# Performance work log

Measured on AMD Instinct MI355X. Metric: run time of the kernel, lower is better.

## Reference

```python
import jax, jax.numpy as jnp
import numpy as np

N = 8_388_608        # cohort size (2^23)
T_MAX = 1_000_000    # distinct time values -> ~8 ties per unique time


def setup_inputs() -> dict:
    key = jax.random.key(0)
    k1, k2, k3 = jax.random.split(key, 3)
    x = jax.random.normal(k1, (N,), dtype=jnp.float32)  # risk scores
    times = jax.random.randint(k2, (N,), 0, T_MAX).astype(jnp.float32)
    events = (jax.random.uniform(k3, (N,)) < 0.7).astype(jnp.float32)
    target = jnp.stack([times, events], axis=1)  # [N, 2] = [time, event]
    return {"input": x, "target": target}


def _cox_breslow_sqrt_loss(x, target):
    times = target[:, 0]
    events_all = target[:, 1]
    n = x.shape[0]
    # Sort by descending time (risk set = prefix in this ordering).
    sort_idx = jnp.argsort(-times)
    t = times[sort_idx]
    ev = events_all[sort_idx]
    xs = x[sort_idx]
    # Stable prefix log-sum-exp over the risk set.
    log_cum = jax.lax.cumlogsumexp(xs)
    # end_idx[i] = last index of the tie group containing i (groups are
    # contiguous after sorting). Reverse running-min over positions of
    # group-last elements.
    is_last = jnp.concatenate([t[:-1] != t[1:], jnp.ones((1,), dtype=bool)])
    pos = jnp.where(is_last, jnp.arange(n), n)
    end_idx = jnp.flip(jax.lax.cummin(jnp.flip(pos)))
    # Breslow: -sum(x*ev) + sum_groups logcum[group_end] * (#events in group)
    #        == -sum((x - logcum[end_idx]) * ev)
    loss = -jnp.sum((xs - log_cum[end_idx]) * ev)
    # reduction='mean' -> sqrt(loss / n)
    return jnp.sqrt(loss / n)


def reference(input, target):
    return _cox_breslow_sqrt_loss(input, target)
```

## Files before the change

### kernel.cpp

```cpp
#include <hip/hip_runtime.h>
#include <math.h>

#define TMAX 1000000
#define BINW 4096
#define BINSHIFT 12
#define NBIN 245
#define PADN (NBIN * BINW)
#define TILE 8192
#define NTHR 512
#define CAP 36864
#define CURSOR_STRIDE 16
#define BT_STRIDE 8
#define FIXSCALE 65536.0f
#define INV_FIXSCALE (1.0 / 65536.0)

#define OFF_SCAL     0
#define OFF_DONE     16
#define OFF_CURSOR   64
#define OFF_BINTOT   15744
#define OFF_PAYLOAD  31488
#define MEMSET_BYTES 31424
#define NEED_FULL    ((size_t)OFF_PAYLOAD + (size_t)NBIN * CAP * 4)
#define FB_BINTOT    15744
#define FB_CEXCL     17792
#define FB_BEXP      31488
#define FB_BEV       (FB_BEXP + PADN * 4)
#define NEED_MIN     ((size_t)FB_BEV + PADN * 4)

__device__ __forceinline__ int clamp_tau(float t) {
    int tau = (int)t;
    if (tau < 0) tau = 0;
    if (tau >= TMAX) tau = TMAX - 1;
    return tau;
}

__device__ __forceinline__ unsigned enc_payload(float xv, float tv, float ev_f,
                                                int* bin_out, float* exq_out) {
    int tau = clamp_tau(tv);
    *bin_out = tau >> BINSHIFT;
    int fine = tau & (BINW - 1);
    float ex = __expf(xv);
    unsigned bb = __float_as_uint(ex);
    bb = (bb + 0x7FFFu + ((bb >> 16) & 1u)) >> 16;
    *exq_out = __uint_as_float(bb << 16);
    unsigned ev = (ev_f != 0.0f) ? 1u : 0u;
    return (bb << 16) | ((unsigned)fine << 1) | ev;
}

__device__ __forceinline__ void hist1(unsigned long long* hist, unsigned p) {
    float ex = __uint_as_float((p >> 16) << 16);
    unsigned fx = __float2uint_rn(ex * FIXSCALE);
    unsigned long long add = ((unsigned long long)(p & 1u) << 48) | (unsigned long long)fx;
    atomicAdd(&hist[(p >> 1) & (BINW - 1)], add);
}

__device__ __forceinline__ void hist4(unsigned long long* hist, uint4 pv) {
    hist1(hist, pv.x); hist1(hist, pv.y); hist1(hist, pv.z); hist1(hist, pv.w);
}

__global__ __launch_bounds__(NTHR) void k_scatter(const float* __restrict__ x,
                                                  const float* __restrict__ tgt,
                                                  unsigned* __restrict__ cursor,
                                                  unsigned* __restrict__ payload,
                                                  double* __restrict__ bintot,
                                                  double* __restrict__ evx_out, int n) {
    __shared__ unsigned cnt[256];
    __shared__ unsigned lpre[256];
    __shared__ unsigned base_s[256];
    __shared__ float binsum[256];
    __shared__ unsigned pay_lds[TILE];
    __shared__ unsigned char binof[TILE];
    __shared__ unsigned wtot_s[8];
    __shared__ double wpart[8];
    const int t = threadIdx.x;
    const int lane = t & 63;
    const int wv = t >> 6;
    if (t < 256) { cnt[t] = 0; binsum[t] = 0.0f; }
    __syncthreads();

    const int tile0 = blockIdx.x * TILE;
    const int tilecount = min(TILE, n - tile0);
    unsigned pay[16], meta[16];
    double evx = 0.0;

    if (tilecount == TILE) {
        const float4* x4 = (const float4*)x;
        const float4* t4 = (const float4*)tgt;
        const int g0 = blockIdx.x * (TILE / 4);
#pragma unroll
        for (int j = 0; j < 4; ++j) {
            const int g = g0 + j * NTHR + t;
            float4 xv = x4[g];
            float4 ta = t4[2 * g];
            float4 tb = t4[2 * g + 1];
            float xs[4] = {xv.x, xv.y, xv.z, xv.w};
            float ts[4] = {ta.x, ta.z, tb.x, tb.z};
            float es[4] = {ta.y, ta.w, tb.y, tb.w};
#pragma unroll
            for (int e = 0; e < 4; ++e) {
                int bin; float exq;
                unsigned p = enc_payload(xs[e], ts[e], es[e], &bin, &exq);
                unsigned r = atomicAdd(&cnt[bin], 1u);
                atomicAdd(&binsum[bin], exq);
                pay[4 * j + e] = p;
                meta[4 * j + e] = ((unsigned)bin << 13) | r;
                if (p & 1) evx += (double)xs[e];
            }
        }
    } else {
        const float2* tg2 = (const float2*)tgt;
#pragma unroll
        for (int j = 0; j < 16; ++j) {
            int idx = tile0 + j * NTHR + t;
            if (idx < n) {
                float xv = x[idx];
                float2 te = tg2[idx];
                int bin; float exq;
                unsigned p = enc_payload(xv, te.x, te.y, &bin, &exq);
                unsigned r = atomicAdd(&cnt[bin], 1u);
                atomicAdd(&binsum[bin], exq);
                pay[j] = p;
                meta[j] = ((unsigned)bin << 13) | r;
                if (p & 1) evx += (double)xv;
            } else {
                meta[j] = 0xFFFFFFFFu;
            }
        }
    }
    __syncthreads();

    const unsigned c = (t < 256) ? cnt[t] : 0u;
    unsigned pfx = c;
#pragma unroll
    for (int d = 1; d < 64; d <<= 1) {
        unsigned u = __shfl_up(pfx, d);
        if (lane >= d) pfx += u;
    }
    if (lane == 63) wtot_s[wv] = pfx;
    __syncthreads();
    unsigned wbase = 0;
    if (t < 256) {
        for (int w = 0; w < wv; ++w) wbase += wtot_s[w];
    }
    const unsigned excl = (t < 256) ? (wbase + pfx - c) : 0u;
    if (t < 256) lpre[t] = excl;

    if (t < NBIN && c) base_s[t] = atomicAdd(&cursor[t * CURSOR_STRIDE], c);

    if (t < NBIN) {
        for (unsigned k = excl; k < excl + c; ++k) binof[k] = (unsigned char)t;
    }
    __syncthreads();

#pragma unroll
    for (int j = 0; j < 16; ++j) {
        if (meta[j] != 0xFFFFFFFFu) {
            unsigned bin = meta[j] >> 13;
            pay_lds[lpre[bin] + (meta[j] & 0x1FFFu)] = pay[j];
        }
    }
    __syncthreads();

    if (tilecount == TILE) {
#pragma unroll 4
        for (int kk = 0; kk < TILE / NTHR; ++kk) {
            const int k = kk * NTHR + t;
            unsigned b = binof[k];
            unsigned pos = base_s[b] + ((unsigned)k - lpre[b]);
            if (pos < CAP) payload[(size_t)b * CAP + pos] = pay_lds[k];
        }
    } else {
        for (int k = t; k < tilecount; k += NTHR) {
            unsigned b = binof[k];
            unsigned pos = base_s[b] + ((unsigned)k - lpre[b]);
            if (pos < CAP) payload[(size_t)b * CAP + pos] = pay_lds[k];
        }
    }

    if (t < NBIN) {
        float s = binsum[t];
        if (s != 0.0f) unsafeAtomicAdd(&bintot[t * BT_STRIDE], (double)s);
    }

#pragma unroll
    for (int d = 32; d > 0; d >>= 1) {
        double u = __shfl_down(evx, d);
        if (lane + d < 64) evx += u;
    }
    if (lane == 0) wpart[wv] = evx;
    __syncthreads();
    if (t == 0) {
        double s = 0.0;
        for (int w = 0; w < 8; ++w) s += wpart[w];
        atomicAdd(evx_out, s);
    }
}

__global__ __launch_bounds__(1024) void k_fused(const unsigned* __restrict__ payload,
                                                const unsigned* __restrict__ cursor,
                                                const double* __restrict__ bintot,
                                                double* __restrict__ scal,
                                                unsigned* __restrict__ done,
                                                float* __restrict__ out, int n) {
    __shared__ unsigned long long hist[BINW];
    __shared__ double wsumA[16];
    __shared__ double wsum[16];
    __shared__ double bcast;
    const int b = blockIdx.x;
    const int t = threadIdx.x;
    const int lane = t & 63;
    const int wv = t >> 6;

#pragma unroll
    for (int j = 0; j < BINW / 1024; ++j) hist[t + j * 1024] = 0ull;
    __syncthreads();

    unsigned cnt = cursor[b * CURSOR_STRIDE];
    if (cnt > CAP) cnt = CAP;
    const unsigned* seg = payload + (size_t)b * CAP;
    const uint4* seg4 = (const uint4*)seg;
    const unsigned n4 = cnt >> 2;
    unsigned i = t;
    for (; i + 1024 < n4; i += 2048) {
        uint4 a = seg4[i];
        uint4 c4 = seg4[i + 1024];
        hist4(hist, a);
        hist4(hist, c4);
    }
    for (; i < n4; i += 1024) hist4(hist, seg4[i]);
    for (unsigned k = (n4 << 2) + t; k < cnt; k += 1024) hist1(hist, seg[k]);
    __syncthreads();

    double ce = 0.0;
    for (int idx = b + 1 + t; idx < NBIN; idx += 1024) ce += bintot[idx * BT_STRIDE];
#pragma unroll
    for (int d = 32; d > 0; d >>= 1) {
        double u = __shfl_down(ce, d);
        if (lane + d < 64) ce += u;
    }
    if (lane == 0) wsumA[wv] = ce;
    __syncthreads();
    if (t == 0) {
        double s = 0.0;
        for (int w = 0; w < 16; ++w) s += wsumA[w];
        bcast = s;
    }
    __syncthreads();
    const double cexcl = bcast;

    const int tb = t * 4;
    double vex[4];
    unsigned vcnt[4];
    double segtot = 0.0;
#pragma unroll
    for (int j = 0; j < 4; ++j) {
        unsigned long long h = hist[tb + j];
        vex[j] = (double)(h & 0xFFFFFFFFFFFFull) * INV_FIXSCALE;
        vcnt[j] = (unsigned)(h >> 48);
        segtot += vex[j];
    }
    double isuf = segtot;
#pragma unroll
    for (int d = 1; d < 64; d <<= 1) {
        double u = __shfl_down(isuf, d);
        if (lane + d < 64) isuf += u;
    }
    if (lane == 0) wsum[wv] = isuf;
    __syncthreads();
    double wexcl = 0.0;
    for (int w = wv + 1; w < 16; ++w) wexcl += wsum[w];

    double run = cexcl + wexcl + (isuf - segtot);
    double local = 0.0;
#pragma unroll
    for (int j = 3; j >= 0; --j) {
        run += vex[j];
        if (vcnt[j]) local += (double)vcnt[j] * log(run);
    }

#pragma unroll
    for (int d = 32; d > 0; d >>= 1) {
        double u = __shfl_down(local, d);
        if (lane + d < 64) local += u;
    }
    if (lane == 0) wsumA[wv] = local;
    __syncthreads();
    if (t == 0) {
        double s = 0.0;
        for (int w = 0; w < 16; ++w) s += wsumA[w];
        unsafeAtomicAdd(&scal[1], s);
        __threadfence();
        unsigned tk = atomicAdd(done, 1u);
        if (tk == NBIN - 1) {
            double ld = unsafeAtomicAdd(&scal[1], 0.0);
            double loss = ld - scal[0];
            if (loss < 0.0) loss = 0.0;
            out[0] = (float)sqrt(loss / (double)n);
        }
    }
}

__global__ void k_accum(const float* __restrict__ x, const float* __restrict__ tgt,
                        float* __restrict__ bexp, float* __restrict__ bev,
                        double* __restrict__ evx_out, int ngroups) {
    double local = 0.0;
    const int nt = gridDim.x * blockDim.x;
    const int tid = blockIdx.x * blockDim.x + threadIdx.x;
    const float4* x4 = (const float4*)x;
    const float4* t4 = (const float4*)tgt;
    for (int g = tid; g < ngroups; g += nt) {
        float4 xv = x4[g];
        float4 ta = t4[2 * g];
        float4 tb = t4[2 * g + 1];
        float xs[4] = {xv.x, xv.y, xv.z, xv.w};
        float ts[4] = {ta.x, ta.z, tb.x, tb.z};
        float es[4] = {ta.y, ta.w, tb.y, tb.w};
#pragma unroll
        for (int j = 0; j < 4; ++j) {
            int tau = clamp_tau(ts[j]);
            unsafeAtomicAdd(&bexp[tau], __expf(xs[j]));
            if (es[j] != 0.0f) unsafeAtomicAdd(&bev[tau], es[j]);
            local += (double)(es[j] * xs[j]);
        }
    }
    __shared__ double sm[256];
    sm[threadIdx.x] = local;
    __syncthreads();
    for (int s = 128; s > 0; s >>= 1) {
        if (threadIdx.x < s) sm[threadIdx.x] += sm[threadIdx.x + s];
        __syncthreads();
    }
    if (threadIdx.x == 0) atomicAdd(evx_out, sm[0]);
}

__global__ void k_chunksum(const float* __restrict__ bexp, double* __restrict__ bintot) {
    const int b = blockIdx.x;
    double local = 0.0;
    for (int i = b * BINW + (int)threadIdx.x; i < (b + 1) * BINW; i += (int)blockDim.x)
        local += (double)bexp[i];
    __shared__ double sm[256];
    sm[threadIdx.x] = local;
    __syncthreads();
    for (int s = 128; s > 0; s >>= 1) {
        if (threadIdx.x < s) sm[threadIdx.x] += sm[threadIdx.x + s];
        __syncthreads();
    }
    if (threadIdx.x == 0) bintot[b] = sm[0];
}

__global__ __launch_bounds__(256) void k_scanbins(const double* __restrict__ bintot,
                                                  double* __restrict__ cexcl) {
    __shared__ double sm[256];
    const int t = threadIdx.x;
    sm[t] = (t < NBIN) ? bintot[t] : 0.0;
    __syncthreads();
    for (int d = 1; d < 256; d <<= 1) {
        double v = (t + d < 256) ? sm[t + d] : 0.0;
        __syncthreads();
        sm[t] += v;
        __syncthreads();
    }
    double e = (t + 1 < 256) ? sm[t + 1] : 0.0;
    __syncthreads();
    cexcl[t] = e;
}

__global__ __launch_bounds__(256) void k_logdot_g(const float* __restrict__ bexp,
                                                  const float* __restrict__ bev,
                                                  const double* __restrict__ cexcl,
                                                  double* __restrict__ logdot) {
    const int b = blockIdx.x;
    const int t = threadIdx.x;
    const float4* e4 = (const float4*)(bexp + b * BINW + t * 16);
    const float4* v4 = (const float4*)(bev + b * BINW + t * 16);
    float ve[16], vv[16];
#pragma unroll
    for (int q = 0; q < 4; ++q) {
        float4 a = e4[q], bb = v4[q];
        ve[4 * q] = a.x; ve[4 * q + 1] = a.y; ve[4 * q + 2] = a.z; ve[4 * q + 3] = a.w;
        vv[4 * q] = bb.x; vv[4 * q + 1] = bb.y; vv[4 * q + 2] = bb.z; vv[4 * q + 3] = bb.w;
    }
    double segtot = 0.0;
#pragma unroll
    for (int j = 0; j < 16; ++j) segtot += (double)ve[j];
    __shared__ double sm[256];
    sm[t] = segtot;
    __syncthreads();
    for (int d = 1; d < 256; d <<= 1) {
        double v = (t + d < 256) ? sm[t + d] : 0.0;
        __syncthreads();
        sm[t] += v;
        __syncthreads();
    }
    double excl = (t < 255) ? sm[t + 1] : 0.0;
    double run = cexcl[b] + excl;
    double local = 0.0;
#pragma unroll
    for (int j = 15; j >= 0; --j) {
        run += (double)ve[j];
        if (vv[j] > 0.0f) local += (double)vv[j] * log(run);
    }
    __syncthreads();
    sm[t] = local;
    __syncthreads();
    for (int s = 128; s > 0; s >>= 1) {
        if (t < s) sm[t] += sm[t + s];
        __syncthreads();
    }
    if (t == 0) atomicAdd(logdot, sm[0]);
}

__global__ void k_final(const double* __restrict__ scal, float* __restrict__ out, int n) {
    if (threadIdx.x == 0 && blockIdx.x == 0) {
        double loss = scal[1] - scal[0];
        if (loss < 0.0) loss = 0.0;
        out[0] = (float)sqrt(loss / (double)n);
    }
}

extern "C" void kernel_launch(void* const* d_in, const int* in_sizes, int n_in,
                              void* d_out, int out_size, void* d_ws, size_t ws_size,
                              hipStream_t stream) {
    const float* x = (const float*)d_in[0];
    const float* tgt = (const float*)d_in[1];
    float* out = (float*)d_out;
    int n = in_sizes[0];

    char* ws = (char*)d_ws;
    double* scal = (double*)(ws + OFF_SCAL);
    unsigned* done = (unsigned*)(ws + OFF_DONE);
    unsigned* cursor = (unsigned*)(ws + OFF_CURSOR);
    double* bintot = (double*)(ws + OFF_BINTOT);
    unsigned* payload = (unsigned*)(ws + OFF_PAYLOAD);

    if (ws_size >= NEED_FULL) {
        hipMemsetAsync(ws, 0, MEMSET_BYTES, stream);
        const int nblk = (n + TILE - 1) / TILE;
        k_scatter<<<nblk, NTHR, 0, stream>>>(x, tgt, cursor, payload, bintot, scal, n);
        k_fused<<<NBIN, 1024, 0, stream>>>(payload, cursor, bintot, scal, done, out, n);
    } else if (ws_size >= NEED_MIN) {
        float* bexp = (float*)(ws + FB_BEXP);
        float* bev = (float*)(ws + FB_BEV);
        double* bintotF = (double*)(ws + FB_BINTOT);
        double* cexclF = (double*)(ws + FB_CEXCL);
        hipMemsetAsync(ws, 0, NEED_MIN, stream);
        k_accum<<<2048, 256, 0, stream>>>(x, tgt, bexp, bev, scal, n / 4);
        k_chunksum<<<NBIN, 256, 0, stream>>>(bexp, bintotF);
        k_scanbins<<<1, 256, 0, stream>>>(bintotF, cexclF);
        k_logdot_g<<<NBIN, 256, 0, stream>>>(bexp, bev, cexclF, scal + 1);
        k_final<<<1, 1, 0, stream>>>(scal, out, n);
    }
}
```

Measured before the change: 187.2 us.

## Replace 64-bit fixed-point histogram with float LDS atomics and second payload pass

The fused kernel now builds a float histogram of exp values with float LDS atomicAdd instead of packed 64-bit fixed-point count+sum atomics. It then writes the suffix sums back to LDS and re-reads each bin's payload segment, computing log per event element rather than count*log per time bucket. The scatter kernel drops the per-element shared float atomic for bin sums and instead sums each bin's range from the LDS tile. The change trades cheaper atomics for an extra global read of the payload, and roughly eight times more double-precision log calls, since there are about eight ties per time value.

Result: slower. 228.8 us (+22.2%).

```diff
diff --git a/kernel.cpp b/kernel.cpp
--- a/kernel.cpp
+++ b/kernel.cpp
@@ -11,8 +11,6 @@
 #define CAP 36864
 #define CURSOR_STRIDE 16
 #define BT_STRIDE 8
-#define FIXSCALE 65536.0f
-#define INV_FIXSCALE (1.0 / 65536.0)
 
 #define OFF_SCAL     0
 #define OFF_DONE     16
@@ -34,28 +32,19 @@
     return tau;
 }
 
-__device__ __forceinline__ unsigned enc_payload(float xv, float tv, float ev_f,
-                                                int* bin_out, float* exq_out) {
+__device__ __forceinline__ unsigned enc_payload(float xv, float tv, float ev_f, int* bin_out) {
     int tau = clamp_tau(tv);
     *bin_out = tau >> BINSHIFT;
     int fine = tau & (BINW - 1);
     float ex = __expf(xv);
     unsigned bb = __float_as_uint(ex);
     bb = (bb + 0x7FFFu + ((bb >> 16) & 1u)) >> 16;
-    *exq_out = __uint_as_float(bb << 16);
     unsigned ev = (ev_f != 0.0f) ? 1u : 0u;
     return (bb << 16) | ((unsigned)fine << 1) | ev;
 }
 
-__device__ __forceinline__ void hist1(unsigned long long* hist, unsigned p) {
-    float ex = __uint_as_float((p >> 16) << 16);
-    unsigned fx = __float2uint_rn(ex * FIXSCALE);
-    unsigned long long add = ((unsigned long long)(p & 1u) << 48) | (unsigned long long)fx;
-    atomicAdd(&hist[(p >> 1) & (BINW - 1)], add);
-}
-
-__device__ __forceinline__ void hist4(unsigned long long* hist, uint4 pv) {
-    hist1(hist, pv.x); hist1(hist, pv.y); hist1(hist, pv.z); hist1(hist, pv.w);
+__device__ __forceinline__ float dec_exp(unsigned p) {
+    return __uint_as_float((p >> 16) << 16);
 }
 
 __global__ __launch_bounds__(NTHR) void k_scatter(const float* __restrict__ x,
@@ -67,7 +56,6 @@
     __shared__ unsigned cnt[256];
     __shared__ unsigned lpre[256];
     __shared__ unsigned base_s[256];
-    __shared__ float binsum[256];
     __shared__ unsigned pay_lds[TILE];
     __shared__ unsigned char binof[TILE];
     __shared__ unsigned wtot_s[8];
@@ -75,7 +63,7 @@
     const int t = threadIdx.x;
     const int lane = t & 63;
     const int wv = t >> 6;
-    if (t < 256) { cnt[t] = 0; binsum[t] = 0.0f; }
+    if (t < 256) cnt[t] = 0;
     __syncthreads();
 
     const int tile0 = blockIdx.x * TILE;
@@ -98,10 +86,9 @@
             float es[4] = {ta.y, ta.w, tb.y, tb.w};
 #pragma unroll
             for (int e = 0; e < 4; ++e) {
-                int bin; float exq;
-                unsigned p = enc_payload(xs[e], ts[e], es[e], &bin, &exq);
+                int bin;
+                unsigned p = enc_payload(xs[e], ts[e], es[e], &bin);
                 unsigned r = atomicAdd(&cnt[bin], 1u);
-                atomicAdd(&binsum[bin], exq);
                 pay[4 * j + e] = p;
                 meta[4 * j + e] = ((unsigned)bin << 13) | r;
                 if (p & 1) evx += (double)xs[e];
@@ -115,10 +102,9 @@
             if (idx < n) {
                 float xv = x[idx];
                 float2 te = tg2[idx];
-                int bin; float exq;
-                unsigned p = enc_payload(xv, te.x, te.y, &bin, &exq);
+                int bin;
+                unsigned p = enc_payload(xv, te.x, te.y, &bin);
                 unsigned r = atomicAdd(&cnt[bin], 1u);
-                atomicAdd(&binsum[bin], exq);
                 pay[j] = p;
                 meta[j] = ((unsigned)bin << 13) | r;
                 if (p & 1) evx += (double)xv;
@@ -160,6 +146,12 @@
         }
     }
     __syncthreads();
+
+    if (t < NBIN && c) {
+        float s = 0.0f;
+        for (unsigned k = excl; k < excl + c; ++k) s += dec_exp(pay_lds[k]);
+        unsafeAtomicAdd(&bintot[t * BT_STRIDE], (double)s);
+    }
 
     if (tilecount == TILE) {
 #pragma unroll 4
@@ -177,11 +169,6 @@
         }
     }
 
-    if (t < NBIN) {
-        float s = binsum[t];
-        if (s != 0.0f) unsafeAtomicAdd(&bintot[t * BT_STRIDE], (double)s);
-    }
-
 #pragma unroll
     for (int d = 32; d > 0; d >>= 1) {
         double u = __shfl_down(evx, d);
@@ -202,9 +189,9 @@
                                                 double* __restrict__ scal,
                                                 unsigned* __restrict__ done,
                                                 float* __restrict__ out, int n) {
-    __shared__ unsigned long long hist[BINW];
+    __shared__ float fexp[BINW];
+    __shared__ double wsum[16];
     __shared__ double wsumA[16];
-    __shared__ double wsum[16];
     __shared__ double bcast;
     const int b = blockIdx.x;
     const int t = threadIdx.x;
@@ -212,7 +199,7 @@
     const int wv = t >> 6;
 
 #pragma unroll
-    for (int j = 0; j < BINW / 1024; ++j) hist[t + j * 1024] = 0ull;
+    for (int j = 0; j < BINW / 1024; ++j) fexp[t + j * 1024] = 0.0f;
     __syncthreads();
 
     unsigned cnt = cursor[b * CURSOR_STRIDE];
@@ -220,15 +207,29 @@
     const unsigned* seg = payload + (size_t)b * CAP;
     const uint4* seg4 = (const uint4*)seg;
     const unsigned n4 = cnt >> 2;
+
     unsigned i = t;
     for (; i + 1024 < n4; i += 2048) {
         uint4 a = seg4[i];
         uint4 c4 = seg4[i + 1024];
-        hist4(hist, a);
-        hist4(hist, c4);
-    }
-    for (; i < n4; i += 1024) hist4(hist, seg4[i]);
-    for (unsigned k = (n4 << 2) + t; k < cnt; k += 1024) hist1(hist, seg[k]);
+        atomicAdd(&fexp[(a.x >> 1) & (BINW - 1)], dec_exp(a.x));
+        atomicAdd(&fexp[(a.y >> 1) & (BINW - 1)], dec_exp(a.y));
+        atomicAdd(&fexp[(a.z >> 1) & (BINW - 1)], dec_exp(a.z));
+        atomicAdd(&fexp[(a.w >> 1) & (BINW - 1)], dec_exp(a.w));
+        atomicAdd(&fexp[(c4.x >> 1) & (BINW - 1)], dec_exp(c4.x));
+        atomicAdd(&fexp[(c4.y >> 1) & (BINW - 1)], dec_exp(c4.y));
+        atomicAdd(&fexp[(c4.z >> 1) & (BINW - 1)], dec_exp(c4.z));
+        atomicAdd(&fexp[(c4.w >> 1) & (BINW - 1)], dec_exp(c4.w));
+    }
+    for (; i < n4; i += 1024) {
+        uint4 a = seg4[i];
+        atomicAdd(&fexp[(a.x >> 1) & (BINW - 1)], dec_exp(a.x));
+        atomicAdd(&fexp[(a.y >> 1) & (BINW - 1)], dec_exp(a.y));
+        atomicAdd(&fexp[(a.z >> 1) & (BINW - 1)], dec_exp(a.z));
+        atomicAdd(&fexp[(a.w >> 1) & (BINW - 1)], dec_exp(a.w));
+    }
+    for (unsigned k = (n4 << 2) + t; k < cnt; k += 1024)
+        atomicAdd(&fexp[(seg[k] >> 1) & (BINW - 1)], dec_exp(seg[k]));
     __syncthreads();
 
     double ce = 0.0;
@@ -249,16 +250,8 @@
     const double cexcl = bcast;
 
     const int tb = t * 4;
-    double vex[4];
-    unsigned vcnt[4];
-    double segtot = 0.0;
-#pragma unroll
-    for (int j = 0; j < 4; ++j) {
-        unsigned long long h = hist[tb + j];
-        vex[j] = (double)(h & 0xFFFFFFFFFFFFull) * INV_FIXSCALE;
-        vcnt[j] = (unsigned)(h >> 48);
-        segtot += vex[j];
-    }
+    float v0 = fexp[tb], v1 = fexp[tb + 1], v2 = fexp[tb + 2], v3 = fexp[tb + 3];
+    double segtot = (double)v0 + (double)v1 + (double)v2 + (double)v3;
     double isuf = segtot;
 #pragma unroll
     for (int d = 1; d < 64; d <<= 1) {
@@ -269,13 +262,41 @@
     __syncthreads();
     double wexcl = 0.0;
     for (int w = wv + 1; w < 16; ++w) wexcl += wsum[w];
-
-    double run = cexcl + wexcl + (isuf - segtot);
+    double after = cexcl + wexcl + (isuf - segtot);
+    double s3 = after + (double)v3;
+    double s2 = s3 + (double)v2;
+    double s1 = s2 + (double)v1;
+    double s0 = s1 + (double)v0;
+    fexp[tb]     = (float)s0;
+    fexp[tb + 1] = (float)s1;
+    fexp[tb + 2] = (float)s2;
+    fexp[tb + 3] = (float)s3;
+    __syncthreads();
+
     double local = 0.0;
-#pragma unroll
-    for (int j = 3; j >= 0; --j) {
-        run += vex[j];
-        if (vcnt[j]) local += (double)vcnt[j] * log(run);
+    i = t;
+    for (; i + 1024 < n4; i += 2048) {
+        uint4 a = seg4[i];
+        uint4 c4 = seg4[i + 1024];
+        if (a.x & 1) local += log((double)fexp[(a.x >> 1) & (BINW - 1)]);
+        if (a.y & 1) local += log((double)fexp[(a.y >> 1) & (BINW - 1)]);
+        if (a.z & 1) local += log((double)fexp[(a.z >> 1) & (BINW - 1)]);
+        if (a.w & 1) local += log((double)fexp[(a.w >> 1) & (BINW - 1)]);
+        if (c4.x & 1) local += log((double)fexp[(c4.x >> 1) & (BINW - 1)]);
+        if (c4.y & 1) local += log((double)fexp[(c4.y >> 1) & (BINW - 1)]);
+        if (c4.z & 1) local += log((double)fexp[(c4.z >> 1) & (BINW - 1)]);
+        if (c4.w & 1) local += log((double)fexp[(c4.w >> 1) & (BINW - 1)]);
+    }
+    for (; i < n4; i += 1024) {
+        uint4 a = seg4[i];
+        if (a.x & 1) local += log((double)fexp[(a.x >> 1) & (BINW - 1)]);
+        if (a.y & 1) local += log((double)fexp[(a.y >> 1) & (BINW - 1)]);
+        if (a.z & 1) local += log((double)fexp[(a.z >> 1) & (BINW - 1)]);
+        if (a.w & 1) local += log((double)fexp[(a.w >> 1) & (BINW - 1)]);
+    }
+    for (unsigned k = (n4 << 2) + t; k < cnt; k += 1024) {
+        unsigned p = seg[k];
+        if (p & 1) local += log((double)fexp[(p >> 1) & (BINW - 1)]);
     }
 
 #pragma unroll
```
